# Kernel optimization log

Measured on AMD Instinct MI355X. Metric: run time of the kernel, lower is better.

Reference implementation:

```python
import jax, jax.numpy as jnp
import numpy as np

B, L_R, H = 8, 128, 512
CTX_LEN, STATE_NUM, ACT_NUM = 256, 32, 32
L_SRC = CTX_LEN + STATE_NUM + ACT_NUM
N_VOCAB = 32000
N_TOPIC = 4096


def setup_inputs() -> dict:
    key = jax.random.key(0)
    ks = jax.random.split(key, 9)
    return {
        "dec_out": jax.random.normal(ks[0], (B, L_R, H), jnp.float32),
        "src_hidden": jax.random.normal(ks[1], (B, L_SRC, H), jnp.float32),
        "W_gen": jax.random.normal(ks[2], (H, N_VOCAB), jnp.float32) * 0.02,
        "b_gen": jnp.zeros((N_VOCAB,), jnp.float32),
        "src_mask": jax.random.randint(ks[3], (B, 1, L_SRC), 0, 2, jnp.int32),
        "context": jax.random.randint(ks[4], (B, CTX_LEN), 0, N_VOCAB, jnp.int32),
        "tp": jax.random.randint(ks[5], (B, STATE_NUM), 0, N_TOPIC, jnp.int32),
        "action": jax.random.randint(ks[6], (B, ACT_NUM), 0, N_TOPIC, jnp.int32),
        "loc2glo": jax.random.randint(ks[7], (N_TOPIC,), 0, N_VOCAB, jnp.int32),
    }


def _scatter_vocab(prob, idx):
    # prob: [L_r, L_seg], idx: [L_seg] global-vocab ids -> [L_r, n_vocab]
    # duplicate indices accumulate, matching torch scatter_add / one-hot bmm
    return jnp.zeros((prob.shape[0], N_VOCAB), prob.dtype).at[:, idx].add(prob)


def reference(dec_out, src_hidden, W_gen, b_gen, src_mask, context, tp, action, loc2glo):
    # gen logits: [B, L_r, n_vocab]
    gen_logit = jnp.einsum("blh,hv->blv", dec_out, W_gen) + b_gen
    # copy logits over concatenated source: [B, L_r, L_src]
    copy_logit = jnp.einsum("blh,bsh->bls", dec_out, src_hidden)
    copy_logit = jnp.where(src_mask == 0, jnp.float32(-1e9), copy_logit)
    logits = jnp.concatenate([gen_logit, copy_logit], axis=-1)
    logits = logits * (H ** -0.5)  # op.scale_prj
    probs = jax.nn.softmax(logits, axis=-1)

    gen_prob = probs[:, :, :N_VOCAB]
    copy_ctx = probs[:, :, N_VOCAB:N_VOCAB + CTX_LEN]
    copy_tp = probs[:, :, N_VOCAB + CTX_LEN:N_VOCAB + CTX_LEN + STATE_NUM]
    copy_ar = probs[:, :, N_VOCAB + CTX_LEN + STATE_NUM:]

    scatter = jax.vmap(_scatter_vocab)
    ctx_prob = scatter(copy_ctx, context)                 # replaces one-hot bmm
    tp_prob = scatter(copy_tp, loc2glo[tp])               # scatter_add via loc2glo gather
    ar_prob = scatter(copy_ar, loc2glo[action])

    return gen_prob + ctx_prob + tp_prob + ar_prob
```

## Files before the change

### kernel.cpp

```cpp
#include <hip/hip_runtime.h>
#include <stdint.h>
#include <stddef.h>

#define NV    32000
#define HDIM  512
#define LSRC  320
#define MROWS 1024
#define SCALEF 0.044194173824159216f

typedef unsigned short u16;
typedef unsigned int   u32;
typedef __attribute__((ext_vector_type(8))) short short8;
typedef __attribute__((ext_vector_type(4))) float floatx4;

__device__ __forceinline__ u16 f2bf(float f) {
  u32 x = __float_as_uint(f);
  return (u16)((x + 0x7fffu + ((x >> 16) & 1u)) >> 16);
}

__global__ __launch_bounds__(256) void k_convA(const float* __restrict__ dec,
                                               u16* __restrict__ Ab,
                                               float* __restrict__ rowSum) {
  if (blockIdx.x == 0) {
    ((float4*)rowSum)[threadIdx.x] = (float4){0.f, 0.f, 0.f, 0.f};
  }
  int t = blockIdx.x * 256 + threadIdx.x;
  int o = t * 8;
  int tile = o >> 12;
  int mt = tile >> 4, kt = tile & 15;
  int mi = (o & 4095) >> 5, ki = o & 31;
  const float* s = dec + (size_t)(mt * 128 + mi) * HDIM + kt * 32 + ki;
  float4 a = ((const float4*)s)[0];
  float4 b = ((const float4*)s)[1];
  union { u16 h[8]; uint4 v; } pk;
  pk.h[0] = f2bf(a.x); pk.h[1] = f2bf(a.y); pk.h[2] = f2bf(a.z); pk.h[3] = f2bf(a.w);
  pk.h[4] = f2bf(b.x); pk.h[5] = f2bf(b.y); pk.h[6] = f2bf(b.z); pk.h[7] = f2bf(b.w);
  *(uint4*)(Ab + o) = pk.v;
}

__global__ __launch_bounds__(256) void k_convW(const float* __restrict__ W,
                                               u16* __restrict__ Wb) {
  __shared__ u16 lds[128 * 36];
  int tileId = blockIdx.x;
  int nt = tileId >> 4, kt = tileId & 15;
  int t = threadIdx.x;
  const float* src = W + (size_t)kt * 32 * NV + (size_t)nt * 128;
#pragma unroll
  for (int i = 0; i < 4; ++i) {
    int f = t + 256 * i;
    int kin = f >> 5, n4 = f & 31;
    float4 v = *(const float4*)(src + (size_t)kin * NV + n4 * 4);
    int base = (n4 * 4) * 36 + kin;
    lds[base]       = f2bf(v.x);
    lds[base + 36]  = f2bf(v.y);
    lds[base + 72]  = f2bf(v.z);
    lds[base + 108] = f2bf(v.w);
  }
  __syncthreads();
  u16* dst = Wb + (size_t)tileId * 4096;
#pragma unroll
  for (int j = 0; j < 2; ++j) {
    int o = t * 8 + j * 2048;
    int ni = o >> 5, ki0 = o & 31;
    const u16* p = &lds[ni * 36 + ki0];
    uint2 x = *(const uint2*)p;
    uint2 y = *(const uint2*)(p + 4);
    uint4 v; v.x = x.x; v.y = x.y; v.z = y.x; v.w = y.y;
    *(uint4*)(dst + o) = v;
  }
}

__global__ __launch_bounds__(256) void k_convS(const float* __restrict__ srch,
                                               u16* __restrict__ Sb) {
  int t = blockIdx.x * 256 + threadIdx.x;
  int o = t * 8;
  int ki = o & 31;
  int ni = (o >> 5) & 127;
  int kt = (o >> 12) & 15;
  int r  = o >> 16;
  int tile = r % 3, b = r / 3;
  int s = tile * 128 + ni;
  uint4 v;
  if (s < LSRC) {
    const float* p = srch + ((size_t)b * LSRC + s) * HDIM + kt * 32 + ki;
    float4 a = ((const float4*)p)[0];
    float4 c = ((const float4*)p)[1];
    union { u16 h[8]; uint4 u; } pk;
    pk.h[0] = f2bf(a.x); pk.h[1] = f2bf(a.y); pk.h[2] = f2bf(a.z); pk.h[3] = f2bf(a.w);
    pk.h[4] = f2bf(c.x); pk.h[5] = f2bf(c.y); pk.h[6] = f2bf(c.z); pk.h[7] = f2bf(c.w);
    v = pk.u;
  } else {
    v = (uint4){0u, 0u, 0u, 0u};
  }
  *(uint4*)(Sb + o) = v;
}

__global__ __launch_bounds__(256) void k_gemm(const u16* __restrict__ Ab,
                                              const u16* __restrict__ Wb,
                                              const u16* __restrict__ Sb,
                                              const float* __restrict__ bgen,
                                              const int* __restrict__ mask,
                                              u16* __restrict__ wsE,
                                              float* __restrict__ wsCopy,
                                              float* __restrict__ rowSum) {
  int bid = blockIdx.x;
  int x = (bid >> 3) & 7;
  int y = ((bid >> 6) << 3) | (bid & 7);
  if (y >= 253) return;
  int t = threadIdx.x;
  int wid = t >> 6, lane = t & 63;
  int wm = wid >> 1, wn = wid & 1;
  int quad = lane >> 4, l16 = lane & 15;
  const u16* Ag = Ab + (size_t)x * (16 * 4096)
                + (wm * 64 + l16) * 32 + quad * 8;
  const u16* Bbase = (y < 250) ? (Wb + (size_t)y * (16 * 4096))
                               : (Sb + (size_t)(x * 3 + (y - 250)) * (16 * 4096));
  const u16* Bg = Bbase + (wn * 64 + l16) * 32 + quad * 8;
  floatx4 acc[4][4];
#pragma unroll
  for (int i = 0; i < 4; ++i)
#pragma unroll
    for (int j = 0; j < 4; ++j) acc[i][j] = (floatx4){0.f, 0.f, 0.f, 0.f};

  short8 aF[2][4], bF[3][4];
#pragma unroll
  for (int i = 0; i < 4; ++i) {
    aF[0][i] = *(const short8*)(Ag + i * 512);
    bF[0][i] = *(const short8*)(Bg + i * 512);
    bF[1][i] = *(const short8*)(Bg + 4096 + i * 512);
  }
#pragma unroll
  for (int kt = 0; kt < 16; ++kt) {
    if (kt < 15) {
      const u16* ap = Ag + (kt + 1) * 4096;
#pragma unroll
      for (int i = 0; i < 4; ++i) aF[(kt + 1) & 1][i] = *(const short8*)(ap + i * 512);
    }
    if (kt < 14) {
      const u16* bp = Bg + (kt + 2) * 4096;
#pragma unroll
      for (int i = 0; i < 4; ++i) bF[(kt + 2) % 3][i] = *(const short8*)(bp + i * 512);
    }
    __builtin_amdgcn_sched_barrier(0);
#pragma unroll
    for (int mt = 0; mt < 4; ++mt)
#pragma unroll
      for (int nt = 0; nt < 4; ++nt)
        acc[mt][nt] = __builtin_amdgcn_mfma_f32_16x16x32_bf16(aF[kt & 1][mt],
                                                              bF[kt % 3][nt],
                                                              acc[mt][nt], 0, 0, 0);
  }

  int row0 = x * 128 + wm * 64;
  if (y < 250) {
    int col0 = y * 128 + wn * 64;
    float bg[4];
#pragma unroll
    for (int nt = 0; nt < 4; ++nt) bg[nt] = bgen[col0 + nt * 16 + l16];
#pragma unroll
    for (int mt = 0; mt < 4; ++mt) {
      float rs[4] = {0.f, 0.f, 0.f, 0.f};
#pragma unroll
      for (int nt = 0; nt < 4; ++nt) {
        int col = col0 + nt * 16 + l16;
#pragma unroll
        for (int r = 0; r < 4; ++r) {
          int row = row0 + mt * 16 + quad * 4 + r;
          float e = __expf((acc[mt][nt][r] + bg[nt]) * SCALEF);
          wsE[(size_t)row * NV + col] = f2bf(e);
          rs[r] += e;
        }
      }
#pragma unroll
      for (int r = 0; r < 4; ++r) {
        float v = rs[r];
        v += __shfl_xor(v, 1, 64);
        v += __shfl_xor(v, 2, 64);
        v += __shfl_xor(v, 4, 64);
        v += __shfl_xor(v, 8, 64);
        if (l16 == 0) atomicAdd(&rowSum[row0 + mt * 16 + quad * 4 + r], v);
      }
    }
  } else {
    int b = x;
    int sBase = (y - 250) * 128 + wn * 64;
#pragma unroll
    for (int mt = 0; mt < 4; ++mt) {
      float rs[4] = {0.f, 0.f, 0.f, 0.f};
#pragma unroll
      for (int nt = 0; nt < 4; ++nt) {
        int s = sBase + nt * 16 + l16;
        int valid = (s < LSRC);
        int m = valid ? mask[b * LSRC + s] : 0;
#pragma unroll
        for (int r = 0; r < 4; ++r) {
          int row = row0 + mt * 16 + quad * 4 + r;
          float e = m ? __expf(acc[mt][nt][r] * SCALEF) : 0.f;
          if (valid) wsCopy[row * LSRC + s] = e;
          rs[r] += e;
        }
      }
#pragma unroll
      for (int r = 0; r < 4; ++r) {
        float v = rs[r];
        v += __shfl_xor(v, 1, 64);
        v += __shfl_xor(v, 2, 64);
        v += __shfl_xor(v, 4, 64);
        v += __shfl_xor(v, 8, 64);
        if (l16 == 0) atomicAdd(&rowSum[row0 + mt * 16 + quad * 4 + r], v);
      }
    }
  }
}

__global__ __launch_bounds__(256) void k_norm(const u16* __restrict__ wsE,
                                              const float* __restrict__ wsCopy,
                                              const float* __restrict__ rowSum,
                                              const int* __restrict__ context,
                                              const int* __restrict__ tp,
                                              const int* __restrict__ action,
                                              const int* __restrict__ loc2glo,
                                              float* __restrict__ out) {
  int r = blockIdx.x, b = r >> 7;
  float inv = 1.0f / rowSum[r];
  const uint2* src = (const uint2*)(wsE + (size_t)r * NV);
  float4* dst = (float4*)(out + (size_t)r * NV);
  for (int c = threadIdx.x; c < NV / 4; c += 256) {
    uint2 v = src[c];
    float4 o;
    o.x = __uint_as_float(v.x << 16) * inv;
    o.y = __uint_as_float(v.x & 0xffff0000u) * inv;
    o.z = __uint_as_float(v.y << 16) * inv;
    o.w = __uint_as_float(v.y & 0xffff0000u) * inv;
    dst[c] = o;
  }
  __syncthreads();
  int t = threadIdx.x;
  float* op = out + (size_t)r * NV;
  atomicAdd(op + context[b * 256 + t], wsCopy[r * LSRC + t] * inv);
  if (t < 32) {
    atomicAdd(op + loc2glo[tp[b * 32 + t]],     wsCopy[r * LSRC + 256 + t] * inv);
    atomicAdd(op + loc2glo[action[b * 32 + t]], wsCopy[r * LSRC + 288 + t] * inv);
  }
}

extern "C" void kernel_launch(void* const* d_in, const int* in_sizes, int n_in,
                              void* d_out, int out_size, void* d_ws, size_t ws_size,
                              hipStream_t stream) {
  const float* dec  = (const float*)d_in[0];
  const float* srch = (const float*)d_in[1];
  const float* Wg   = (const float*)d_in[2];
  const float* bg   = (const float*)d_in[3];
  const int*   mask = (const int*)d_in[4];
  const int*   ctx  = (const int*)d_in[5];
  const int*   tp   = (const int*)d_in[6];
  const int*   act  = (const int*)d_in[7];
  const int*   l2g  = (const int*)d_in[8];
  float* out = (float*)d_out;

  char* ws = (char*)d_ws;
  u16*   Wb      = (u16*)(ws);
  u16*   wsE     = (u16*)(ws + 32768000);
  u16*   Ab      = (u16*)(ws + 98304000);
  float* wsCopy  = (float*)(ws + 99352576);
  float* rowSum  = (float*)(ws + 100663296);
  u16*   Sb      = (u16*)(ws + 100667392);

  hipLaunchKernelGGL(k_convA, dim3(256), dim3(256), 0, stream, dec, Ab, rowSum);
  hipLaunchKernelGGL(k_convW, dim3(4000), dim3(256), 0, stream, Wg, Wb);
  hipLaunchKernelGGL(k_convS, dim3(768), dim3(256), 0, stream, srch, Sb);
  hipLaunchKernelGGL(k_gemm, dim3(2048), dim3(256), 0, stream, Ab, Wb, Sb, bg, mask,
                     wsE, wsCopy, rowSum);
  hipLaunchKernelGGL(k_norm, dim3(MROWS), dim3(256), 0, stream, wsE, wsCopy, rowSum,
                     ctx, tp, act, l2g, out);
}
```

Measured before the change: 342.4 us.

## Stage GEMM tiles through LDS with async global_load_lds double buffering

Replaces the per-wave direct global-to-register operand loads in the fused GEMM with async global_load_lds copies into double-buffered shared memory tiles. Each wave now loads a distinct slice once and all waves read their fragments from LDS, so redundant global traffic across waves is removed. The cost is a block-wide barrier every k-step and added LDS reads. Prefetch depth also drops from two tiles ahead to one for B.

```diff
diff --git a/kernel.cpp b/kernel.cpp
--- a/kernel.cpp
+++ b/kernel.cpp
@@ -16,6 +16,12 @@
 __device__ __forceinline__ u16 f2bf(float f) {
   u32 x = __float_as_uint(f);
   return (u16)((x + 0x7fffu + ((x >> 16) & 1u)) >> 16);
+}
+
+typedef __attribute__((address_space(1))) void gvoid;
+typedef __attribute__((address_space(3))) void lvoid;
+__device__ __forceinline__ void cp16(const u16* g, u16* l) {
+  __builtin_amdgcn_global_load_lds((gvoid*)g, (lvoid*)l, 16, 0, 0);
 }
 
 __global__ __launch_bounds__(256) void k_convA(const float* __restrict__ dec,
@@ -103,6 +109,8 @@
                                               u16* __restrict__ wsE,
                                               float* __restrict__ wsCopy,
                                               float* __restrict__ rowSum) {
+  __shared__ u16 As[2][4096];
+  __shared__ u16 Bs[2][4096];
   int bid = blockIdx.x;
   int x = (bid >> 3) & 7;
   int y = ((bid >> 6) << 3) | (bid & 7);
@@ -111,44 +119,54 @@
   int wid = t >> 6, lane = t & 63;
   int wm = wid >> 1, wn = wid & 1;
   int quad = lane >> 4, l16 = lane & 15;
-  const u16* Ag = Ab + (size_t)x * (16 * 4096)
-                + (wm * 64 + l16) * 32 + quad * 8;
-  const u16* Bbase = (y < 250) ? (Wb + (size_t)y * (16 * 4096))
-                               : (Sb + (size_t)(x * 3 + (y - 250)) * (16 * 4096));
-  const u16* Bg = Bbase + (wn * 64 + l16) * 32 + quad * 8;
+
+  const u16* At = Ab + (size_t)x * (16 * 4096);
+  const u16* Bt = (y < 250) ? (Wb + (size_t)y * (16 * 4096))
+                            : (Sb + (size_t)(x * 3 + (y - 250)) * (16 * 4096));
+  const u16* Ag0 = At + wid * 1024 + lane * 8;
+  const u16* Bg0 = Bt + wid * 1024 + lane * 8;
+  u16* Al0 = &As[0][wid * 1024];
+  u16* Bl0 = &Bs[0][wid * 1024];
+
   floatx4 acc[4][4];
 #pragma unroll
   for (int i = 0; i < 4; ++i)
 #pragma unroll
     for (int j = 0; j < 4; ++j) acc[i][j] = (floatx4){0.f, 0.f, 0.f, 0.f};
 
-  short8 aF[2][4], bF[3][4];
-#pragma unroll
-  for (int i = 0; i < 4; ++i) {
-    aF[0][i] = *(const short8*)(Ag + i * 512);
-    bF[0][i] = *(const short8*)(Bg + i * 512);
-    bF[1][i] = *(const short8*)(Bg + 4096 + i * 512);
-  }
+  cp16(Ag0,        Al0);
+  cp16(Ag0 + 512,  Al0 + 512);
+  cp16(Bg0,        Bl0);
+  cp16(Bg0 + 512,  Bl0 + 512);
+  __syncthreads();
+
+  int cb = 0;
 #pragma unroll
   for (int kt = 0; kt < 16; ++kt) {
+    int nb = cb ^ 1;
     if (kt < 15) {
-      const u16* ap = Ag + (kt + 1) * 4096;
-#pragma unroll
-      for (int i = 0; i < 4; ++i) aF[(kt + 1) & 1][i] = *(const short8*)(ap + i * 512);
+      const u16* ag = Ag0 + (kt + 1) * 4096;
+      const u16* bg = Bg0 + (kt + 1) * 4096;
+      cp16(ag,       &As[nb][wid * 1024]);
+      cp16(ag + 512, &As[nb][wid * 1024 + 512]);
+      cp16(bg,       &Bs[nb][wid * 1024]);
+      cp16(bg + 512, &Bs[nb][wid * 1024 + 512]);
     }
-    if (kt < 14) {
-      const u16* bp = Bg + (kt + 2) * 4096;
-#pragma unroll
-      for (int i = 0; i < 4; ++i) bF[(kt + 2) % 3][i] = *(const short8*)(bp + i * 512);
-    }
-    __builtin_amdgcn_sched_barrier(0);
+    short8 aR[4], bR[4];
 #pragma unroll
     for (int mt = 0; mt < 4; ++mt)
+      aR[mt] = *(const short8*)&As[cb][(wm * 64 + mt * 16 + l16) * 32 + quad * 8];
+#pragma unroll
+    for (int nt = 0; nt < 4; ++nt)
+      bR[nt] = *(const short8*)&Bs[cb][(wn * 64 + nt * 16 + l16) * 32 + quad * 8];
+#pragma unroll
+    for (int mt = 0; mt < 4; ++mt)
 #pragma unroll
       for (int nt = 0; nt < 4; ++nt)
-        acc[mt][nt] = __builtin_amdgcn_mfma_f32_16x16x32_bf16(aF[kt & 1][mt],
-                                                              bF[kt % 3][nt],
+        acc[mt][nt] = __builtin_amdgcn_mfma_f32_16x16x32_bf16(aR[mt], bR[nt],
                                                               acc[mt][nt], 0, 0, 0);
+    __syncthreads();
+    cb = nb;
   }
 
   int row0 = x * 128 + wm * 64;
```

Result: no change. 344.3 us (+0.6%).
